# Performance work log

Measured on AMD Instinct MI355X. Metric: run time of the kernel, lower is better.

Reference implementation:

```python
import jax, jax.numpy as jnp
import numpy as np

B, D, S, O = 32768, 1024, 64, 4  # batch, feature_dim, n_subjects, n_outputs


def setup_inputs() -> dict:
    key = jax.random.key(0)
    kx, ks, kw, kb = jax.random.split(key, 4)
    x = jax.random.normal(kx, (B, D), dtype=jnp.float32)          # backbone features
    subject_ids = jax.random.randint(ks, (B,), 0, S)              # per-sample head id
    W = jax.random.normal(kw, (S, D, O), dtype=jnp.float32) / np.float32(np.sqrt(D))
    b = jax.random.normal(kb, (S, O), dtype=jnp.float32) * 0.01
    return {"x": x, "subject_ids": subject_ids, "W": W, "b": b}


def reference(x, subject_ids, W, b):
    # Vectorized form of the per-subject loop:
    #   for sid in unique(subject_ids): outputs[idxs] = heads[sid](features[idxs])
    # Each head is Linear(D, O): out[i] = x[i] @ W[sid[i]] + b[sid[i]].
    Wg = jnp.take(W, subject_ids, axis=0)   # [B, D, O] gathered per-sample weights
    bg = jnp.take(b, subject_ids, axis=0)   # [B, O]
    return jnp.einsum('bd,bdo->bo', x, Wg) + bg
```

## Files before the change

kernel.cpp:

```cpp
#include <hip/hip_runtime.h>

constexpr int B = 32768;
constexpr int D = 1024;
constexpr int S = 64;
constexpr int O = 4;


constexpr int CHUNKS      = 16;
constexpr int CHUNK       = B / CHUNKS;
constexpr int SEG         = CHUNK / 4;
constexpr int MAIN_BLOCKS = S * CHUNKS;

__global__ __launch_bounds__(256)
__attribute__((amdgpu_waves_per_eu(4, 4)))
void main_kernel(
    const float* __restrict__ x,
    const int*   __restrict__ sid,
    const float* __restrict__ W,
    const float* __restrict__ bias,
    float*       __restrict__ out)
{
    __shared__ float Wt[O * D];
    __shared__ int   list[4][SEG];

    const int t    = threadIdx.x;
    const int lane = t & 63;
    const int wave = t >> 6;
    const int s    = blockIdx.x >> 4;
    const int c    = blockIdx.x & 15;
    const int q    = lane >> 4;

    {
        const float4* Wp = (const float4*)(W + (size_t)s * (D * O));
        #pragma unroll
        for (int r = 0; r < 4; ++r) {
            const int d = r * 256 + t;
            const float4 w4 = Wp[d];
            Wt[0 * D + d] = w4.x;
            Wt[1 * D + d] = w4.y;
            Wt[2 * D + d] = w4.z;
            Wt[3 * D + d] = w4.w;
        }
    }

    const int seg = c * CHUNK + wave * SEG;
    int cnt = 0;
    #pragma unroll
    for (int r = 0; r < 8; ++r) {
        const int i = seg + r * 64 + lane;
        const bool m = (sid[i] == s);
        const unsigned long long mask = __ballot(m);
        const int rank = __popcll(mask & ((1ull << lane) - 1ull));
        if (m) list[wave][cnt + rank] = i;
        cnt += __popcll(mask);
    }

    __syncthreads();
    if (cnt == 0) return;

    const float   bb  = bias[(s << 2) + q];
    const float4* Wt4 = (const float4*)Wt;

#define LOADX(XB, ROW)                                                         \
    {                                                                          \
        const float4* xr = (const float4*)(x + ((size_t)(ROW) << 10));         \
        _Pragma("unroll")                                                      \
        for (int j = 0; j < 4; ++j) XB[j] = xr[64 * j + lane];                 \
    }

#define COMPUTE(XC, ROW)                                                       \
    {                                                                          \
        float a0 = 0.f, a1 = 0.f, a2 = 0.f, a3 = 0.f;                          \
        _Pragma("unroll")                                                      \
        for (int j = 0; j < 4; ++j) {                                          \
            const float4 xv = XC[j];                                           \
            const float4 w0 = Wt4[0 * 256 + 64 * j + lane];                    \
            const float4 w1 = Wt4[1 * 256 + 64 * j + lane];                    \
            const float4 w2 = Wt4[2 * 256 + 64 * j + lane];                    \
            const float4 w3 = Wt4[3 * 256 + 64 * j + lane];                    \
            a0 += xv.x * w0.x; a1 += xv.x * w1.x;                              \
            a2 += xv.x * w2.x; a3 += xv.x * w3.x;                              \
            a0 += xv.y * w0.y; a1 += xv.y * w1.y;                              \
            a2 += xv.y * w2.y; a3 += xv.y * w3.y;                              \
            a0 += xv.z * w0.z; a1 += xv.z * w1.z;                              \
            a2 += xv.z * w2.z; a3 += xv.z * w3.z;                              \
            a0 += xv.w * w0.w; a1 += xv.w * w1.w;                              \
            a2 += xv.w * w2.w; a3 += xv.w * w3.w;                              \
        }                                                                      \
        _Pragma("unroll")                                                      \
        for (int m = 16; m <= 32; m <<= 1) {                                   \
            a0 += __shfl_xor(a0, m, 64);                                       \
            a1 += __shfl_xor(a1, m, 64);                                       \
            a2 += __shfl_xor(a2, m, 64);                                       \
            a3 += __shfl_xor(a3, m, 64);                                       \
        }                                                                      \
        float v = (q == 0) ? a0 : (q == 1) ? a1 : (q == 2) ? a2 : a3;          \
        _Pragma("unroll")                                                      \
        for (int m = 1; m <= 8; m <<= 1)                                       \
            v += __shfl_xor(v, m, 64);                                         \
        if ((lane & 15) == 0)                  \
            out[((size_t)(ROW) << 2) + q] = v + bb;                            \
    }

    float4 xbA[4], xbB[4];
    int rowA = __builtin_amdgcn_readfirstlane(list[wave][0]);
    LOADX(xbA, rowA)

    int k = 0;
    #pragma unroll 1
    while (k + 2 <= cnt) {
        const int rowB = __builtin_amdgcn_readfirstlane(list[wave][k + 1]);
        LOADX(xbB, rowB)
        COMPUTE(xbA, rowA)
        if (k + 2 < cnt) {
            const int rowN = __builtin_amdgcn_readfirstlane(list[wave][k + 2]);
            LOADX(xbA, rowN)
            COMPUTE(xbB, rowB)
            rowA = rowN;
        } else {
            COMPUTE(xbB, rowB)
        }
        k += 2;
    }
    if (k < cnt)
        COMPUTE(xbA, rowA)

#undef LOADX
#undef COMPUTE
}

extern "C" void kernel_launch(void* const* d_in, const int* in_sizes, int n_in,
                              void* d_out, int out_size, void* d_ws, size_t ws_size,
                              hipStream_t stream) {
    const float* x    = (const float*)d_in[0];
    const int*   sid  = (const int*)d_in[1];
    const float* W    = (const float*)d_in[2];
    const float* bias = (const float*)d_in[3];
    float* out = (float*)d_out;

    main_kernel<<<MAIN_BLOCKS, 256, 0, stream>>>(x, sid, W, bias, out);
}
```

Before: 206.2 us.

## Balance rows across waves, raise chunk count, deepen x prefetch with nontemporal loads

Raises the chunk count from 16 to 64, giving four times more blocks, each scanning a smaller slice of subject ids. Instead of each wave processing only the matches it found itself, the per-wave counts are shared through LDS and matched rows are striped across all four waves, which balances their work. Row indices are stored as 16-bit values, x rows are read with nontemporal loads, and the next x row is prefetched mid-compute for a two-deep software pipeline. The cost is four times more redundant W staging into LDS, a branchy index lookup per row, and a stray unused label left in the code.

```diff
diff --git a/kernel.cpp b/kernel.cpp
--- a/kernel.cpp
+++ b/kernel.cpp
@@ -6,10 +6,12 @@
 constexpr int O = 4;
 
 
-constexpr int CHUNKS      = 16;
+constexpr int CHUNKS      = 64;
 constexpr int CHUNK       = B / CHUNKS;
-constexpr int SEG         = CHUNK / 4;
+constexpr int WSEG        = CHUNK / 4;
 constexpr int MAIN_BLOCKS = S * CHUNKS;
+
+typedef float f4 __attribute__((ext_vector_type(4)));
 
 __global__ __launch_bounds__(256)
 __attribute__((amdgpu_waves_per_eu(4, 4)))
@@ -20,22 +22,23 @@
     const float* __restrict__ bias,
     float*       __restrict__ out)
 {
-    __shared__ float Wt[O * D];
-    __shared__ int   list[4][SEG];
+    __shared__ float          Wt[O * D];
+    __shared__ unsigned short wlist[4][WSEG];
+    __shared__ int            wcnt[4];
 
     const int t    = threadIdx.x;
     const int lane = t & 63;
     const int wave = t >> 6;
-    const int s    = blockIdx.x >> 4;
-    const int c    = blockIdx.x & 15;
+    const int s    = blockIdx.x >> 6;
+    const int c    = blockIdx.x & 63;
     const int q    = lane >> 4;
 
     {
-        const float4* Wp = (const float4*)(W + (size_t)s * (D * O));
+        const f4* Wp = (const f4*)(W + (size_t)s * (D * O));
         #pragma unroll
         for (int r = 0; r < 4; ++r) {
             const int d = r * 256 + t;
-            const float4 w4 = Wp[d];
+            const f4 w4 = Wp[d];
             Wt[0 * D + d] = w4.x;
             Wt[1 * D + d] = w4.y;
             Wt[2 * D + d] = w4.z;
@@ -43,41 +46,70 @@
         }
     }
 
-    const int seg = c * CHUNK + wave * SEG;
+    const int seg = c * CHUNK + wave * WSEG;
     int cnt = 0;
     #pragma unroll
-    for (int r = 0; r < 8; ++r) {
+    for (int r = 0; r < 2; ++r) {
         const int i = seg + r * 64 + lane;
         const bool m = (sid[i] == s);
         const unsigned long long mask = __ballot(m);
         const int rank = __popcll(mask & ((1ull << lane) - 1ull));
-        if (m) list[wave][cnt + rank] = i;
+        if (m) wlist[wave][cnt + rank] = (unsigned short)i;
         cnt += __popcll(mask);
     }
+    if (lane == 0) wcnt[wave] = cnt;
+
+    const float bb = bias[(s << 2) + q];
 
     __syncthreads();
-    if (cnt == 0) return;
 
-    const float   bb  = bias[(s << 2) + q];
-    const float4* Wt4 = (const float4*)Wt;
+    const int c0 = wcnt[0], c1 = wcnt[1], c2 = wcnt[2], c3 = wcnt[3];
+    const int p1 = c0, p2 = c0 + c1, p3 = c0 + c1 + c2;
+    const int total = p3 + c3;
+
+#define ROW_OF(G, DST) do {                                                    \
+        int _g = (G), _r;                                                      \
+        if      (_g < p1) _r = wlist[0][_g];                                   \
+        else if (_g < p2) _r = wlist[1][_g - p1];                              \
+        else if (_g < p3) _r = wlist[2][_g - p2];                              \
+        else              _r = wlist[3][_g - p3];                              \
+        (DST) = __builtin_amdgcn_readfirstlane(_r);                            \
+    } while (0)
 
 #define LOADX(XB, ROW)                                                         \
     {                                                                          \
-        const float4* xr = (const float4*)(x + ((size_t)(ROW) << 10));         \
+        const f4* _xr = (const f4*)(x + ((size_t)(ROW) << 10));                \
         _Pragma("unroll")                                                      \
-        for (int j = 0; j < 4; ++j) XB[j] = xr[64 * j + lane];                 \
+        for (int _j = 0; _j < 4; ++_j)                                         \
+            XB[_j] = __builtin_nontemporal_load(_xr + 64 * _j + lane);         \
     }
 
-#define COMPUTE(XC, ROW)                                                       \
+    int g = wave;
+    if (g >= total) return;
+
+    const f4* Wt4 = (const f4*)Wt;
+
+    float4_dummy_guard: ;
+    f4 xbA[4], xbB[4];
+    int rowC, rowN;
+    ROW_OF(g, rowC);
+    LOADX(xbA, rowC)
+    rowN = rowC;
+    if (g + 4 < total) {
+        ROW_OF(g + 4, rowN);
+        LOADX(xbB, rowN)
+    }
+
+#define PHASE(XC, XN)                                                          \
     {                                                                          \
         float a0 = 0.f, a1 = 0.f, a2 = 0.f, a3 = 0.f;                          \
         _Pragma("unroll")                                                      \
         for (int j = 0; j < 4; ++j) {                                          \
-            const float4 xv = XC[j];                                           \
-            const float4 w0 = Wt4[0 * 256 + 64 * j + lane];                    \
-            const float4 w1 = Wt4[1 * 256 + 64 * j + lane];                    \
-            const float4 w2 = Wt4[2 * 256 + 64 * j + lane];                    \
-            const float4 w3 = Wt4[3 * 256 + 64 * j + lane];                    \
+            const f4 xv = XC[j];                                               \
+            const f4 w0 = Wt4[0 * 256 + 64 * j + lane];   \
+            const f4 w1 = Wt4[1 * 256 + 64 * j + lane];    \
+            const f4 w2 = Wt4[2 * 256 + 64 * j + lane];                        \
+            const f4 w3 = Wt4[3 * 256 + 64 * j + lane];                        \
             a0 += xv.x * w0.x; a1 += xv.x * w1.x;                              \
             a2 += xv.x * w2.x; a3 += xv.x * w3.x;                              \
             a0 += xv.y * w0.y; a1 += xv.y * w1.y;                              \
@@ -86,6 +118,11 @@
             a2 += xv.z * w2.z; a3 += xv.z * w3.z;                              \
             a0 += xv.w * w0.w; a1 += xv.w * w1.w;                              \
             a2 += xv.w * w2.w; a3 += xv.w * w3.w;                              \
+        }                                                                      \
+        int rowP = rowC;                                                       \
+        if (g + 8 < total) {                     \
+            ROW_OF(g + 8, rowP);                                               \
+            LOADX(XC, rowP)                                                    \
         }                                                                      \
         _Pragma("unroll")                                                      \
         for (int m = 16; m <= 32; m <<= 1) {                                   \
@@ -99,34 +136,21 @@
         for (int m = 1; m <= 8; m <<= 1)                                       \
             v += __shfl_xor(v, m, 64);                                         \
         if ((lane & 15) == 0)                  \
-            out[((size_t)(ROW) << 2) + q] = v + bb;                            \
+            out[((size_t)rowC << 2) + q] = v + bb;                             \
+        rowC = rowN; rowN = rowP; g += 4;                                      \
     }
 
-    float4 xbA[4], xbB[4];
-    int rowA = __builtin_amdgcn_readfirstlane(list[wave][0]);
-    LOADX(xbA, rowA)
+    #pragma unroll 1
+    for (;;) {
+        PHASE(xbA, xbB)
+        if (g >= total) break;
+        PHASE(xbB, xbA)
+        if (g >= total) break;
+    }
 
-    int k = 0;
-    #pragma unroll 1
-    while (k + 2 <= cnt) {
-        const int rowB = __builtin_amdgcn_readfirstlane(list[wave][k + 1]);
-        LOADX(xbB, rowB)
-        COMPUTE(xbA, rowA)
-        if (k + 2 < cnt) {
-            const int rowN = __builtin_amdgcn_readfirstlane(list[wave][k + 2]);
-            LOADX(xbA, rowN)
-            COMPUTE(xbB, rowB)
-            rowA = rowN;
-        } else {
-            COMPUTE(xbB, rowB)
-        }
-        k += 2;
-    }
-    if (k < cnt)
-        COMPUTE(xbA, rowA)
-
+#undef PHASE
 #undef LOADX
-#undef COMPUTE
+#undef ROW_OF
 }
 
 extern "C" void kernel_launch(void* const* d_in, const int* in_sizes, int n_in,
```

Measured after the change: 284.2 us. 1.38x slower.
